# Optimization experiments

Measured on AMD Instinct MI355X. Metric: run time of the kernel, lower is better.

## Reference

```python
import jax, jax.numpy as jnp
import numpy as np

C_RADIUS = 20.0  # weighted-L1 ball radius from the cvxpy constraint
EPS = 1e-30


def weighted_l1_ball_projection(q, w, c):
    """Euclidean projection of each row of q onto {x : sum_i w_i*|x_i| <= c}, w>=0.
    Closed-form via sorted breakpoints: x_i = sign(q_i)*max(|q_i| - lam*w_i, 0).
    q, w: [B, D].
    """
    aq = jnp.abs(q)
    wa = w * aq                               # w_i |q_i|
    feasible = jnp.sum(wa, axis=-1) <= c      # already inside the ball
    # breakpoint ratios; coords with w==0 are never clipped -> push to the end
    r = jnp.where(w > 0, aq / jnp.maximum(w, EPS), -jnp.inf)
    order = jnp.argsort(-r, axis=-1)
    wa_s = jnp.take_along_axis(wa, order, axis=-1)
    w2_s = jnp.take_along_axis(w * w, order, axis=-1)
    r_s = jnp.take_along_axis(r, order, axis=-1)
    A = jnp.cumsum(wa_s, axis=-1)             # prefix sums over candidate active sets
    B = jnp.cumsum(w2_s, axis=-1)
    lam_k = (A - c) / jnp.maximum(B, EPS)
    valid = r_s > lam_k                       # active-set condition
    k = jnp.sum(valid, axis=-1)               # size of true active set
    idx = jnp.maximum(k - 1, 0)
    lam = jnp.take_along_axis(lam_k, idx[:, None], axis=-1)[:, 0]
    lam = jnp.where(feasible, 0.0, jnp.maximum(lam, 0.0))
    return jnp.sign(q) * jnp.maximum(aq - lam[:, None] * w, 0.0)


def setup_inputs() -> dict:
    key = jax.random.key(0)
    ks = jax.random.split(key, 8)
    state_dim, action_dim, B = 17, 6, 262144
    # scale state so the weighted-L1 constraint is occasionally active
    state = 4.0 * jax.random.normal(ks[0], (B, state_dim), dtype=jnp.float32)
    def lin(kw, kb, fan_out, fan_in):
        bound = 1.0 / np.sqrt(fan_in)
        W = jax.random.uniform(kw, (fan_out, fan_in), jnp.float32, -bound, bound)
        b = jax.random.uniform(kb, (fan_out,), jnp.float32, -bound, bound)
        return W, b
    l1_w, l1_b = lin(ks[1], ks[2], 400, state_dim)
    l2_w, l2_b = lin(ks[3], ks[4], 300, 400)
    l3_w, l3_b = lin(ks[5], ks[6], action_dim, 300)
    return {"state": state, "l1_w": l1_w, "l1_b": l1_b, "l2_w": l2_w,
            "l2_b": l2_b, "l3_w": l3_w, "l3_b": l3_b, "training": 0}


def reference(state, l1_w, l1_b, l2_w, l2_b, l3_w, l3_b, training):
    max_action = 1.0
    a = jax.nn.relu(state @ l1_w.T + l1_b)
    a = jax.nn.relu(a @ l2_w.T + l2_b)
    scaled_a = max_action * jnp.tanh(a @ l3_w.T + l3_b)  # [B, 6]
    # IS_TRAINING path: QP  min 0.5||x||^2 - q^T x  s.t. sum |x_i * s[11+i]| <= 20
    w = jnp.abs(state[:, 11:17])
    return weighted_l1_ball_projection(scaled_a, w, C_RADIUS)
```

## Files before the change

kernel.cpp:

```cpp
#include <hip/hip_runtime.h>
#include <math.h>

typedef _Float16 half2v __attribute__((ext_vector_type(2)));
typedef __fp16 fp16x2 __attribute__((ext_vector_type(2)));
typedef _Float16 half4 __attribute__((ext_vector_type(4)));
typedef _Float16 half8 __attribute__((ext_vector_type(8)));
typedef float floatx4 __attribute__((ext_vector_type(4)));

#define C_RADIUS 20.0f


__global__ void actor_prep(const float* __restrict__ w1, const float* __restrict__ b1,
                           const float* __restrict__ w2, const float* __restrict__ b2,
                           const float* __restrict__ w3, const float* __restrict__ b3,
                           _Float16* __restrict__ ws) {
  int gid = blockIdx.x * 256 + threadIdx.x;
  if (gid >= 19072) return;
  half8 hv;
  _Float16* dst;
  if (gid < 1792) {
    int l = gid & 63, tn = gid >> 6;
    int n = tn * 16 + (l & 15);
    int kc = 8 * (l >> 4);
#pragma unroll
    for (int e = 0; e < 8; ++e) {
      int k = kc + e;
      float v = 0.f;
      if (n < 400) {
        if (k < 17) v = w1[n * 17 + k];
        else if (k == 17) v = b1[n];
      }
      hv[e] = (_Float16)v;
    }
    dst = ws + gid * 8;
  } else if (gid < 1792 + 16640) {
    int g = gid - 1792;
    int l = g & 63, t = g >> 6;
    int ks = t % 13, tn = t / 13;
    int n = tn * 16 + (l & 15);
    int kc = ks * 32 + 8 * (l >> 4);
#pragma unroll
    for (int e = 0; e < 8; ++e) {
      int k = kc + e;
      float v = 0.f;
      if (n < 300) {
        if (k < 400) v = w2[n * 400 + k];
        else if (k == 400) v = b2[n];
      }
      hv[e] = (_Float16)v;
    }
    dst = ws + 14336 + g * 8;
  } else {
    int g = gid - 1792 - 16640;
    int l = g & 63, ks = g >> 6;
    int n = l & 15;
    int kc = ks * 32 + 8 * (l >> 4);
#pragma unroll
    for (int e = 0; e < 8; ++e) {
      int k = kc + e;
      float v = 0.f;
      if (n < 6) {
        if (k < 300) v = w3[n * 300 + k];
        else if (k == 300) v = b3[n];
      }
      hv[e] = (_Float16)v;
    }
    dst = ws + 147456 + g * 8;
  }
  *reinterpret_cast<half8*>(dst) = hv;
}

#define LD1 424
#define LD2 328
#define LDS_ 40

#define MFMA32(A, B, C) C = __builtin_amdgcn_mfma_f32_16x16x32_f16(A, B, C, 0, 0, 0)

__device__ __forceinline__ half4 pack4(float v0, float v1, float v2, float v3) {
  fp16x2 a = __builtin_amdgcn_cvt_pkrtz(v0, v1);
  fp16x2 b = __builtin_amdgcn_cvt_pkrtz(v2, v3);
  half2v a2 = __builtin_bit_cast(half2v, a);
  half2v b2 = __builtin_bit_cast(half2v, b);
  return __builtin_shufflevector(a2, b2, 0, 1, 2, 3);
}

__device__ __forceinline__ float fast_tanh(float x) {
  float e = __expf(2.0f * x);
  return 1.0f - 2.0f / (e + 1.0f);
}

__global__ __launch_bounds__(512, 4) void actor_fused(const float* __restrict__ state,
                                                      const _Float16* __restrict__ ws,
                                                      float* __restrict__ out) {
  __shared__ __align__(16) _Float16 aL[64 * LD1];
  __shared__ __align__(16) _Float16 stateF[64 * LDS_];
  __shared__ float z3L[64 * 8];
  __shared__ __align__(16) float outL[64 * 6];
  __shared__ float wvL[64 * 6];

  const int tid = threadIdx.x;
  const int lane = tid & 63;
  const int w = tid >> 6;
  const int r15 = lane & 15;
  const int c4 = lane >> 4;
  const int row0 = blockIdx.x * 64;

  for (int i = tid; i < 1088; i += 512) {
    int r = i / 17, c = i - r * 17;
    stateF[r * LDS_ + c] = (_Float16)state[row0 * 17 + i];
  }
  for (int i = tid; i < 64 * 23; i += 512) {
    int r = i / 23, c = 17 + (i - r * 23);
    stateF[r * LDS_ + c] = (c == 17) ? (_Float16)1.0f : (_Float16)0.0f;
  }
  for (int i = tid; i < 1024; i += 512) {
    int r = i >> 4, c = i & 15;
    aL[r * LD1 + 400 + c] = (c == 0) ? (_Float16)1.0f : (_Float16)0.0f;
  }
  if (tid < 384) {
    int r = tid / 6, c = tid - r * 6;
    wvL[tid] = fabsf(state[(row0 + r) * 17 + 11 + c]);
  }
  __syncthreads();

  {
    half8 S[4];
#pragma unroll
    for (int m = 0; m < 4; ++m)
      S[m] = *reinterpret_cast<const half8*>(&stateF[(16 * m + r15) * LDS_ + 8 * c4]);
    const half8* W1f = reinterpret_cast<const half8*>(ws);
#pragma unroll
    for (int t = 0; t < 4; ++t) {
      int tn = w + 8 * t;
      if (tn < 25) {
        half8 aW = W1f[tn * 64 + lane];
        floatx4 acc[4];
#pragma unroll
        for (int m = 0; m < 4; ++m) {
          acc[m] = (floatx4){0.f, 0.f, 0.f, 0.f};
          MFMA32(aW, S[m], acc[m]);
        }
        int n0 = tn * 16 + 4 * c4;
#pragma unroll
        for (int m = 0; m < 4; ++m) {
          half4 hv = pack4(fmaxf(acc[m][0], 0.f), fmaxf(acc[m][1], 0.f),
                           fmaxf(acc[m][2], 0.f), fmaxf(acc[m][3], 0.f));
          *reinterpret_cast<half4*>(&aL[(16 * m + r15) * LD1 + n0]) = hv;
        }
      }
    }
  }
  __syncthreads();

  {
    const half8* W2f = reinterpret_cast<const half8*>(ws + 14336);
    const int nt = (w < 4) ? 3 : 2;
    const int tn0 = (w < 4) ? (w * 3) : (12 + (w - 4) * 2);
    floatx4 acc[4][3];
#pragma unroll
    for (int m = 0; m < 4; ++m)
#pragma unroll
      for (int t = 0; t < 3; ++t) acc[m][t] = (floatx4){0.f, 0.f, 0.f, 0.f};

    half8 bX[3], bY[3];
#pragma unroll
    for (int t = 0; t < 3; ++t)
      if (t < nt) bX[t] = W2f[((tn0 + t) * 13 + 0) * 64 + lane];

#pragma unroll 1
    for (int ks = 0; ks < 13; ++ks) {
      if (ks < 12) {
#pragma unroll
        for (int t = 0; t < 3; ++t)
          if (t < nt) bY[t] = W2f[((tn0 + t) * 13 + ks + 1) * 64 + lane];
      }
      half8 F[4];
#pragma unroll
      for (int m = 0; m < 4; ++m)
        F[m] = *reinterpret_cast<const half8*>(&aL[(16 * m + r15) * LD1 + ks * 32 + 8 * c4]);
#pragma unroll
      for (int t = 0; t < 3; ++t)
        if (t < nt)
#pragma unroll
          for (int m = 0; m < 4; ++m)
            MFMA32(bX[t], F[m], acc[m][t]);
#pragma unroll
      for (int t = 0; t < 3; ++t) bX[t] = bY[t];
    }
    __syncthreads();

#pragma unroll
    for (int t = 0; t < 3; ++t)
      if (t < nt) {
        int n0 = (tn0 + t) * 16 + 4 * c4;
#pragma unroll
        for (int m = 0; m < 4; ++m) {
          float v0 = fmaxf(acc[m][t][0], 0.f), v1 = fmaxf(acc[m][t][1], 0.f);
          float v2 = fmaxf(acc[m][t][2], 0.f), v3 = fmaxf(acc[m][t][3], 0.f);
          if (n0 == 300) v0 = 1.0f;
          half4 hv = pack4(v0, v1, v2, v3);
          *reinterpret_cast<half4*>(&aL[(16 * m + r15) * LD2 + n0]) = hv;
        }
      }
  }
  __syncthreads();

  if (w < 4) {
    const half8* W3f = reinterpret_cast<const half8*>(ws + 147456);
    floatx4 za = (floatx4){0.f, 0.f, 0.f, 0.f};
    floatx4 zb = (floatx4){0.f, 0.f, 0.f, 0.f};
    const int row = 16 * w + r15;
#pragma unroll
    for (int ks = 0; ks < 10; ks += 2) {
      half8 F0 = *reinterpret_cast<const half8*>(&aL[row * LD2 + ks * 32 + 8 * c4]);
      half8 F1 = *reinterpret_cast<const half8*>(&aL[row * LD2 + (ks + 1) * 32 + 8 * c4]);
      MFMA32(W3f[ks * 64 + lane], F0, za);
      MFMA32(W3f[(ks + 1) * 64 + lane], F1, zb);
    }
    floatx4 z = za + zb;
    if (c4 == 0) {
#pragma unroll
      for (int j = 0; j < 4; ++j) z3L[row * 8 + j] = fast_tanh(z[j]);
    } else if (c4 == 1) {
      z3L[row * 8 + 4] = fast_tanh(z[0]);
      z3L[row * 8 + 5] = fast_tanh(z[1]);
    }
  }
  __syncthreads();

  if (tid < 64) {
    const int row = tid;
    float q[6], wv[6], aq[6], wa[6];
    float S = 0.f;
#pragma unroll
    for (int i = 0; i < 6; ++i) {
      q[i] = z3L[row * 8 + i];
      wv[i] = wvL[row * 6 + i];
      aq[i] = fabsf(q[i]);
      wa[i] = wv[i] * aq[i];
      S += wa[i];
    }
    float lam = 0.f;
    if (!(S <= C_RADIUS)) {
      float rr[6], w2s[6], was[6];
#pragma unroll
      for (int i = 0; i < 6; ++i) {
        rr[i] = (wv[i] > 0.f) ? (aq[i] / fmaxf(wv[i], 1e-30f)) : -__builtin_inff();
        w2s[i] = wv[i] * wv[i];
        was[i] = wa[i];
      }
#pragma unroll
      for (int p = 0; p < 5; ++p)
#pragma unroll
        for (int j2 = 0; j2 < 5; ++j2)
          if (j2 < 5 - p) {
            if (rr[j2] < rr[j2 + 1]) {
              float t0 = rr[j2];  rr[j2] = rr[j2 + 1];  rr[j2 + 1] = t0;
              float t1 = w2s[j2]; w2s[j2] = w2s[j2 + 1]; w2s[j2 + 1] = t1;
              float t2 = was[j2]; was[j2] = was[j2 + 1]; was[j2 + 1] = t2;
            }
          }
      float A = 0.f, Bc = 0.f;
      float lamk[6];
      int kc = 0;
#pragma unroll
      for (int i = 0; i < 6; ++i) {
        A += was[i];
        Bc += w2s[i];
        lamk[i] = (A - C_RADIUS) / fmaxf(Bc, 1e-30f);
        if (rr[i] > lamk[i]) ++kc;
      }
      int idx = kc - 1;
      if (idx < 0) idx = 0;
      float lsel = lamk[0];
#pragma unroll
      for (int i = 1; i < 6; ++i)
        if (i == idx) lsel = lamk[i];
      lam = fmaxf(lsel, 0.f);
    }
#pragma unroll
    for (int i = 0; i < 6; ++i) {
      float x = fmaxf(aq[i] - lam * wv[i], 0.f);
      outL[row * 6 + i] = copysignf(x, q[i]);
    }
  }
  __syncthreads();

  if (tid < 96) {
    float4 v = reinterpret_cast<const float4*>(outL)[tid];
    reinterpret_cast<float4*>(out)[blockIdx.x * 96 + tid] = v;
  }
}

extern "C" void kernel_launch(void* const* d_in, const int* in_sizes, int n_in,
                              void* d_out, int out_size, void* d_ws, size_t ws_size,
                              hipStream_t stream) {
  const float* state = (const float*)d_in[0];
  const float* w1 = (const float*)d_in[1];
  const float* b1 = (const float*)d_in[2];
  const float* w2 = (const float*)d_in[3];
  const float* b2 = (const float*)d_in[4];
  const float* w3 = (const float*)d_in[5];
  const float* b3 = (const float*)d_in[6];
  _Float16* ws = (_Float16*)d_ws;
  float* out = (float*)d_out;

  actor_prep<<<75, 256, 0, stream>>>(w1, b1, w2, b2, w3, b3, ws);
  actor_fused<<<4096, 512, 0, stream>>>(state, ws, out);
}
```

Baseline: 97.10 us.

## Trim LDS footprint, fold state into aL pad, raise occupancy, fuse projection tail

Drops the separate stateF, z3L, outL and wvL shared buffers. The state tile now goes into the padding columns of aL, and the layer-2 bias is added in the epilogue instead of through a constant-one column, so the smaller LDS footprint allows launch bounds of 6 blocks. The layer-2 K loop is restructured into ping-pong register buffers, and the first weight load is issued before layer 1. The QP projection now runs directly in the layer-3 wave using shuffles, which removes two barriers and the staged output write, at the cost of higher register pressure and uncoalesced per-row stores.

```diff
diff --git a/kernel.cpp b/kernel.cpp
--- a/kernel.cpp
+++ b/kernel.cpp
@@ -43,10 +43,7 @@
     for (int e = 0; e < 8; ++e) {
       int k = kc + e;
       float v = 0.f;
-      if (n < 300) {
-        if (k < 400) v = w2[n * 400 + k];
-        else if (k == 400) v = b2[n];
-      }
+      if (n < 300 && k < 400) v = w2[n * 400 + k];
       hv[e] = (_Float16)v;
     }
     dst = ws + 14336 + g * 8;
@@ -72,7 +69,6 @@
 
 #define LD1 424
 #define LD2 328
-#define LDS_ 40
 
 #define MFMA32(A, B, C) C = __builtin_amdgcn_mfma_f32_16x16x32_f16(A, B, C, 0, 0, 0)
 
@@ -89,14 +85,11 @@
   return 1.0f - 2.0f / (e + 1.0f);
 }
 
-__global__ __launch_bounds__(512, 4) void actor_fused(const float* __restrict__ state,
+__global__ __launch_bounds__(512, 6) void actor_fused(const float* __restrict__ state,
                                                       const _Float16* __restrict__ ws,
+                                                      const float* __restrict__ b2,
                                                       float* __restrict__ out) {
   __shared__ __align__(16) _Float16 aL[64 * LD1];
-  __shared__ __align__(16) _Float16 stateF[64 * LDS_];
-  __shared__ float z3L[64 * 8];
-  __shared__ __align__(16) float outL[64 * 6];
-  __shared__ float wvL[64 * 6];
 
   const int tid = threadIdx.x;
   const int lane = tid & 63;
@@ -105,29 +98,32 @@
   const int c4 = lane >> 4;
   const int row0 = blockIdx.x * 64;
 
-  for (int i = tid; i < 1088; i += 512) {
-    int r = i / 17, c = i - r * 17;
-    stateF[r * LDS_ + c] = (_Float16)state[row0 * 17 + i];
-  }
-  for (int i = tid; i < 64 * 23; i += 512) {
-    int r = i / 23, c = 17 + (i - r * 23);
-    stateF[r * LDS_ + c] = (c == 17) ? (_Float16)1.0f : (_Float16)0.0f;
-  }
-  for (int i = tid; i < 1024; i += 512) {
-    int r = i >> 4, c = i & 15;
-    aL[r * LD1 + 400 + c] = (c == 0) ? (_Float16)1.0f : (_Float16)0.0f;
-  }
-  if (tid < 384) {
-    int r = tid / 6, c = tid - r * 6;
-    wvL[tid] = fabsf(state[(row0 + r) * 17 + 11 + c]);
+  for (int i = tid; i < 1536; i += 512) {
+    int r = i / 24, c = i - r * 24;
+    float v = 0.f;
+    if (c < 17) v = state[(row0 + r) * 17 + c];
+    else if (c == 17) v = 1.0f;
+    aL[r * LD1 + 400 + c] = (_Float16)v;
   }
   __syncthreads();
+
+  const int nt = (w < 4) ? 3 : 2;
+  const int tn0 = (w < 4) ? (w * 3) : (12 + (w - 4) * 2);
+  const half8* W2f = reinterpret_cast<const half8*>(ws + 14336);
+  half8 bA[3], bB[3];
+#pragma unroll
+  for (int t = 0; t < 3; ++t)
+    if (t < nt) bA[t] = W2f[((tn0 + t) * 13 + 0) * 64 + lane];
 
   {
     half8 S[4];
 #pragma unroll
-    for (int m = 0; m < 4; ++m)
-      S[m] = *reinterpret_cast<const half8*>(&stateF[(16 * m + r15) * LDS_ + 8 * c4]);
+    for (int m = 0; m < 4; ++m) {
+      half8 v = {};
+      if (c4 < 3)
+        v = *reinterpret_cast<const half8*>(&aL[(16 * m + r15) * LD1 + 400 + 8 * c4]);
+      S[m] = v;
+    }
     const half8* W1f = reinterpret_cast<const half8*>(ws);
 #pragma unroll
     for (int t = 0; t < 4; ++t) {
@@ -153,50 +149,65 @@
   __syncthreads();
 
   {
-    const half8* W2f = reinterpret_cast<const half8*>(ws + 14336);
-    const int nt = (w < 4) ? 3 : 2;
-    const int tn0 = (w < 4) ? (w * 3) : (12 + (w - 4) * 2);
     floatx4 acc[4][3];
 #pragma unroll
     for (int m = 0; m < 4; ++m)
 #pragma unroll
       for (int t = 0; t < 3; ++t) acc[m][t] = (floatx4){0.f, 0.f, 0.f, 0.f};
 
-    half8 bX[3], bY[3];
-#pragma unroll
-    for (int t = 0; t < 3; ++t)
-      if (t < nt) bX[t] = W2f[((tn0 + t) * 13 + 0) * 64 + lane];
+    const int n0base = tn0 * 16 + 4 * c4;
+    float4 b2v[3];
+#pragma unroll
+    for (int t = 0; t < 3; ++t) {
+      b2v[t] = make_float4(0.f, 0.f, 0.f, 0.f);
+      int n0 = n0base + 16 * t;
+      if (t < nt && n0 < 300) b2v[t] = *reinterpret_cast<const float4*>(&b2[n0]);
+    }
 
 #pragma unroll 1
-    for (int ks = 0; ks < 13; ++ks) {
-      if (ks < 12) {
+    for (int kp = 0; kp < 6; ++kp) {
+      const int ks0 = 2 * kp, ks1 = 2 * kp + 1, ks2 = 2 * kp + 2;
+#pragma unroll
+      for (int t = 0; t < 3; ++t)
+        if (t < nt) bB[t] = W2f[((tn0 + t) * 13 + ks1) * 64 + lane];
+#pragma unroll
+      for (int m = 0; m < 4; ++m) {
+        half8 F = *reinterpret_cast<const half8*>(&aL[(16 * m + r15) * LD1 + ks0 * 32 + 8 * c4]);
 #pragma unroll
         for (int t = 0; t < 3; ++t)
-          if (t < nt) bY[t] = W2f[((tn0 + t) * 13 + ks + 1) * 64 + lane];
-      }
-      half8 F[4];
-#pragma unroll
-      for (int m = 0; m < 4; ++m)
-        F[m] = *reinterpret_cast<const half8*>(&aL[(16 * m + r15) * LD1 + ks * 32 + 8 * c4]);
+          if (t < nt) MFMA32(bA[t], F, acc[m][t]);
+      }
 #pragma unroll
       for (int t = 0; t < 3; ++t)
-        if (t < nt)
-#pragma unroll
-          for (int m = 0; m < 4; ++m)
-            MFMA32(bX[t], F[m], acc[m][t]);
-#pragma unroll
-      for (int t = 0; t < 3; ++t) bX[t] = bY[t];
-    }
+        if (t < nt) bA[t] = W2f[((tn0 + t) * 13 + ks2) * 64 + lane];
+#pragma unroll
+      for (int m = 0; m < 4; ++m) {
+        half8 F = *reinterpret_cast<const half8*>(&aL[(16 * m + r15) * LD1 + ks1 * 32 + 8 * c4]);
+#pragma unroll
+        for (int t = 0; t < 3; ++t)
+          if (t < nt) MFMA32(bB[t], F, acc[m][t]);
+      }
+    }
+#pragma unroll
+    for (int m = 0; m < 4; ++m) {
+      half8 F = *reinterpret_cast<const half8*>(&aL[(16 * m + r15) * LD1 + 12 * 32 + 8 * c4]);
+#pragma unroll
+      for (int t = 0; t < 3; ++t)
+        if (t < nt) MFMA32(bA[t], F, acc[m][t]);
+    }
+
     __syncthreads();
 
 #pragma unroll
     for (int t = 0; t < 3; ++t)
       if (t < nt) {
-        int n0 = (tn0 + t) * 16 + 4 * c4;
+        int n0 = n0base + 16 * t;
 #pragma unroll
         for (int m = 0; m < 4; ++m) {
-          float v0 = fmaxf(acc[m][t][0], 0.f), v1 = fmaxf(acc[m][t][1], 0.f);
-          float v2 = fmaxf(acc[m][t][2], 0.f), v3 = fmaxf(acc[m][t][3], 0.f);
+          float v0 = fmaxf(acc[m][t][0] + b2v[t].x, 0.f);
+          float v1 = fmaxf(acc[m][t][1] + b2v[t].y, 0.f);
+          float v2 = fmaxf(acc[m][t][2] + b2v[t].z, 0.f);
+          float v3 = fmaxf(acc[m][t][3] + b2v[t].w, 0.f);
           if (n0 == 300) v0 = 1.0f;
           half4 hv = pack4(v0, v1, v2, v3);
           *reinterpret_cast<half4*>(&aL[(16 * m + r15) * LD2 + n0]) = hv;
@@ -218,77 +229,66 @@
       MFMA32(W3f[(ks + 1) * 64 + lane], F1, zb);
     }
     floatx4 z = za + zb;
+    float v4 = __shfl(z[0], r15 + 16, 64);
+    float v5 = __shfl(z[1], r15 + 16, 64);
     if (c4 == 0) {
-#pragma unroll
-      for (int j = 0; j < 4; ++j) z3L[row * 8 + j] = fast_tanh(z[j]);
-    } else if (c4 == 1) {
-      z3L[row * 8 + 4] = fast_tanh(z[0]);
-      z3L[row * 8 + 5] = fast_tanh(z[1]);
-    }
-  }
-  __syncthreads();
-
-  if (tid < 64) {
-    const int row = tid;
-    float q[6], wv[6], aq[6], wa[6];
-    float S = 0.f;
-#pragma unroll
-    for (int i = 0; i < 6; ++i) {
-      q[i] = z3L[row * 8 + i];
-      wv[i] = wvL[row * 6 + i];
-      aq[i] = fabsf(q[i]);
-      wa[i] = wv[i] * aq[i];
-      S += wa[i];
-    }
-    float lam = 0.f;
-    if (!(S <= C_RADIUS)) {
-      float rr[6], w2s[6], was[6];
+      const int grow = row0 + row;
+      float q[6], wv[6], aq[6], wa[6];
+      q[0] = fast_tanh(z[0]); q[1] = fast_tanh(z[1]);
+      q[2] = fast_tanh(z[2]); q[3] = fast_tanh(z[3]);
+      q[4] = fast_tanh(v4);   q[5] = fast_tanh(v5);
+      float S = 0.f;
 #pragma unroll
       for (int i = 0; i < 6; ++i) {
-        rr[i] = (wv[i] > 0.f) ? (aq[i] / fmaxf(wv[i], 1e-30f)) : -__builtin_inff();
-        w2s[i] = wv[i] * wv[i];
-        was[i] = wa[i];
-      }
-#pragma unroll
-      for (int p = 0; p < 5; ++p)
-#pragma unroll
-        for (int j2 = 0; j2 < 5; ++j2)
-          if (j2 < 5 - p) {
-            if (rr[j2] < rr[j2 + 1]) {
-              float t0 = rr[j2];  rr[j2] = rr[j2 + 1];  rr[j2 + 1] = t0;
-              float t1 = w2s[j2]; w2s[j2] = w2s[j2 + 1]; w2s[j2 + 1] = t1;
-              float t2 = was[j2]; was[j2] = was[j2 + 1]; was[j2 + 1] = t2;
+        wv[i] = fabsf(state[grow * 17 + 11 + i]);
+        aq[i] = fabsf(q[i]);
+        wa[i] = wv[i] * aq[i];
+        S += wa[i];
+      }
+      float lam = 0.f;
+      if (!(S <= C_RADIUS)) {
+        float rr[6], w2s[6], was[6];
+#pragma unroll
+        for (int i = 0; i < 6; ++i) {
+          rr[i] = (wv[i] > 0.f) ? (aq[i] / fmaxf(wv[i], 1e-30f)) : -__builtin_inff();
+          w2s[i] = wv[i] * wv[i];
+          was[i] = wa[i];
+        }
+#pragma unroll
+        for (int p = 0; p < 5; ++p)
+#pragma unroll
+          for (int j2 = 0; j2 < 5; ++j2)
+            if (j2 < 5 - p) {
+              if (rr[j2] < rr[j2 + 1]) {
+                float t0 = rr[j2];  rr[j2] = rr[j2 + 1];  rr[j2 + 1] = t0;
+                float t1 = w2s[j2]; w2s[j2] = w2s[j2 + 1]; w2s[j2 + 1] = t1;
+                float t2 = was[j2]; was[j2] = was[j2 + 1]; was[j2 + 1] = t2;
+              }
             }
-          }
-      float A = 0.f, Bc = 0.f;
-      float lamk[6];
-      int kc = 0;
+        float A = 0.f, Bc = 0.f;
+        float lamk[6];
+        int kc = 0;
+#pragma unroll
+        for (int i = 0; i < 6; ++i) {
+          A += was[i];
+          Bc += w2s[i];
+          lamk[i] = (A - C_RADIUS) / fmaxf(Bc, 1e-30f);
+          if (rr[i] > lamk[i]) ++kc;
+        }
+        int idx = kc - 1;
+        if (idx < 0) idx = 0;
+        float lsel = lamk[0];
+#pragma unroll
+        for (int i = 1; i < 6; ++i)
+          if (i == idx) lsel = lamk[i];
+        lam = fmaxf(lsel, 0.f);
+      }
 #pragma unroll
       for (int i = 0; i < 6; ++i) {
-        A += was[i];
-        Bc += w2s[i];
-        lamk[i] = (A - C_RADIUS) / fmaxf(Bc, 1e-30f);
-        if (rr[i] > lamk[i]) ++kc;
-      }
-      int idx = kc - 1;
-      if (idx < 0) idx = 0;
-      float lsel = lamk[0];
-#pragma unroll
-      for (int i = 1; i < 6; ++i)
-        if (i == idx) lsel = lamk[i];
-      lam = fmaxf(lsel, 0.f);
-    }
-#pragma unroll
-    for (int i = 0; i < 6; ++i) {
-      float x = fmaxf(aq[i] - lam * wv[i], 0.f);
-      outL[row * 6 + i] = copysignf(x, q[i]);
-    }
-  }
-  __syncthreads();
-
-  if (tid < 96) {
-    float4 v = reinterpret_cast<const float4*>(outL)[tid];
-    reinterpret_cast<float4*>(out)[blockIdx.x * 96 + tid] = v;
+        float x = fmaxf(aq[i] - lam * wv[i], 0.f);
+        out[grow * 6 + i] = copysignf(x, q[i]);
+      }
+    }
   }
 }
 
@@ -306,5 +306,5 @@
   float* out = (float*)d_out;
 
   actor_prep<<<75, 256, 0, stream>>>(w1, b1, w2, b2, w3, b3, ws);
-  actor_fused<<<4096, 512, 0, stream>>>(state, ws, out);
-}
+  actor_fused<<<4096, 512, 0, stream>>>(state, ws, b2, out);
+}
```

After: 275.7 us. 2.84x slower.

## Shrink LDS footprint and fuse projection into layer-3 waves for higher occupancy

Applied to the files above, without the earlier changes.

Stages state directly into the activation LDS buffer (bias column moved to k=0), drops the separate stateF, z3L, outL and wvL buffers, and trims LD1 so more blocks fit per CU. Occupancy hint rises from 4 to 6. The weighted-L1 projection now runs in the layer-3 waves, using shuffles to gather outputs 4 and 5 and reading weights straight from global memory. This removes two barriers and the LDS round trips. The layer-2 weight prefetch is simplified from double-buffered registers to a single buffer loaded after the MFMAs. That lowers register pressure but exposes more global-load latency, and output stores are now per-thread scattered writes instead of coalesced float4.

```diff
diff --git a/kernel.cpp b/kernel.cpp
--- a/kernel.cpp
+++ b/kernel.cpp
@@ -27,8 +27,8 @@
       int k = kc + e;
       float v = 0.f;
       if (n < 400) {
-        if (k < 17) v = w1[n * 17 + k];
-        else if (k == 17) v = b1[n];
+        if (k == 0) v = b1[n];
+        else if (k <= 17) v = w1[n * 17 + (k - 1)];
       }
       hv[e] = (_Float16)v;
     }
@@ -70,9 +70,8 @@
   *reinterpret_cast<half8*>(dst) = hv;
 }
 
-#define LD1 424
+#define LD1 408
 #define LD2 328
-#define LDS_ 40
 
 #define MFMA32(A, B, C) C = __builtin_amdgcn_mfma_f32_16x16x32_f16(A, B, C, 0, 0, 0)
 
@@ -89,14 +88,10 @@
   return 1.0f - 2.0f / (e + 1.0f);
 }
 
-__global__ __launch_bounds__(512, 4) void actor_fused(const float* __restrict__ state,
+__global__ __launch_bounds__(512, 6) void actor_fused(const float* __restrict__ state,
                                                       const _Float16* __restrict__ ws,
                                                       float* __restrict__ out) {
-  __shared__ __align__(16) _Float16 aL[64 * LD1];
-  __shared__ __align__(16) _Float16 stateF[64 * LDS_];
-  __shared__ float z3L[64 * 8];
-  __shared__ __align__(16) float outL[64 * 6];
-  __shared__ float wvL[64 * 6];
+  __shared__ __align__(16) _Float16 aL[64 * LD1 + 16];
 
   const int tid = threadIdx.x;
   const int lane = tid & 63;
@@ -105,29 +100,27 @@
   const int c4 = lane >> 4;
   const int row0 = blockIdx.x * 64;
 
-  for (int i = tid; i < 1088; i += 512) {
-    int r = i / 17, c = i - r * 17;
-    stateF[r * LDS_ + c] = (_Float16)state[row0 * 17 + i];
-  }
-  for (int i = tid; i < 64 * 23; i += 512) {
-    int r = i / 23, c = 17 + (i - r * 23);
-    stateF[r * LDS_ + c] = (c == 17) ? (_Float16)1.0f : (_Float16)0.0f;
-  }
-  for (int i = tid; i < 1024; i += 512) {
-    int r = i >> 4, c = i & 15;
+  for (int i = tid; i < 2048; i += 512) {
+    int r = i >> 5, c = i & 31;
+    float v = 0.f;
+    if (c == 0) v = 1.0f;
+    else if (c <= 17) v = state[(row0 + r) * 17 + (c - 1)];
+    aL[r * LD1 + c] = (_Float16)v;
+  }
+  {
+    int r = tid >> 3, c = tid & 7;
     aL[r * LD1 + 400 + c] = (c == 0) ? (_Float16)1.0f : (_Float16)0.0f;
   }
-  if (tid < 384) {
-    int r = tid / 6, c = tid - r * 6;
-    wvL[tid] = fabsf(state[(row0 + r) * 17 + 11 + c]);
-  }
+  if (tid < 16) aL[64 * LD1 + tid] = (_Float16)0.0f;
+  __syncthreads();
+
+  half8 S[4];
+#pragma unroll
+  for (int m = 0; m < 4; ++m)
+    S[m] = *reinterpret_cast<const half8*>(&aL[(16 * m + r15) * LD1 + 8 * c4]);
   __syncthreads();
 
   {
-    half8 S[4];
-#pragma unroll
-    for (int m = 0; m < 4; ++m)
-      S[m] = *reinterpret_cast<const half8*>(&stateF[(16 * m + r15) * LDS_ + 8 * c4]);
     const half8* W1f = reinterpret_cast<const half8*>(ws);
 #pragma unroll
     for (int t = 0; t < 4; ++t) {
@@ -162,18 +155,13 @@
 #pragma unroll
       for (int t = 0; t < 3; ++t) acc[m][t] = (floatx4){0.f, 0.f, 0.f, 0.f};
 
-    half8 bX[3], bY[3];
+    half8 bA[3];
 #pragma unroll
     for (int t = 0; t < 3; ++t)
-      if (t < nt) bX[t] = W2f[((tn0 + t) * 13 + 0) * 64 + lane];
+      if (t < nt) bA[t] = W2f[((tn0 + t) * 13 + 0) * 64 + lane];
 
 #pragma unroll 1
     for (int ks = 0; ks < 13; ++ks) {
-      if (ks < 12) {
-#pragma unroll
-        for (int t = 0; t < 3; ++t)
-          if (t < nt) bY[t] = W2f[((tn0 + t) * 13 + ks + 1) * 64 + lane];
-      }
       half8 F[4];
 #pragma unroll
       for (int m = 0; m < 4; ++m)
@@ -183,10 +171,14 @@
         if (t < nt)
 #pragma unroll
           for (int m = 0; m < 4; ++m)
-            MFMA32(bX[t], F[m], acc[m][t]);
-#pragma unroll
-      for (int t = 0; t < 3; ++t) bX[t] = bY[t];
-    }
+            MFMA32(bA[t], F[m], acc[m][t]);
+      if (ks < 12) {
+#pragma unroll
+        for (int t = 0; t < 3; ++t)
+          if (t < nt) bA[t] = W2f[((tn0 + t) * 13 + ks + 1) * 64 + lane];
+      }
+    }
+
     __syncthreads();
 
 #pragma unroll
@@ -218,77 +210,66 @@
       MFMA32(W3f[(ks + 1) * 64 + lane], F1, zb);
     }
     floatx4 z = za + zb;
+    float v4 = __shfl(z[0], r15 + 16, 64);
+    float v5 = __shfl(z[1], r15 + 16, 64);
     if (c4 == 0) {
-#pragma unroll
-      for (int j = 0; j < 4; ++j) z3L[row * 8 + j] = fast_tanh(z[j]);
-    } else if (c4 == 1) {
-      z3L[row * 8 + 4] = fast_tanh(z[0]);
-      z3L[row * 8 + 5] = fast_tanh(z[1]);
-    }
-  }
-  __syncthreads();
-
-  if (tid < 64) {
-    const int row = tid;
-    float q[6], wv[6], aq[6], wa[6];
-    float S = 0.f;
-#pragma unroll
-    for (int i = 0; i < 6; ++i) {
-      q[i] = z3L[row * 8 + i];
-      wv[i] = wvL[row * 6 + i];
-      aq[i] = fabsf(q[i]);
-      wa[i] = wv[i] * aq[i];
-      S += wa[i];
-    }
-    float lam = 0.f;
-    if (!(S <= C_RADIUS)) {
-      float rr[6], w2s[6], was[6];
+      const int grow = row0 + row;
+      float q[6], wv[6], aq[6], wa[6];
+      q[0] = fast_tanh(z[0]); q[1] = fast_tanh(z[1]);
+      q[2] = fast_tanh(z[2]); q[3] = fast_tanh(z[3]);
+      q[4] = fast_tanh(v4);   q[5] = fast_tanh(v5);
+      float S2 = 0.f;
 #pragma unroll
       for (int i = 0; i < 6; ++i) {
-        rr[i] = (wv[i] > 0.f) ? (aq[i] / fmaxf(wv[i], 1e-30f)) : -__builtin_inff();
-        w2s[i] = wv[i] * wv[i];
-        was[i] = wa[i];
-      }
-#pragma unroll
-      for (int p = 0; p < 5; ++p)
-#pragma unroll
-        for (int j2 = 0; j2 < 5; ++j2)
-          if (j2 < 5 - p) {
-            if (rr[j2] < rr[j2 + 1]) {
-              float t0 = rr[j2];  rr[j2] = rr[j2 + 1];  rr[j2 + 1] = t0;
-              float t1 = w2s[j2]; w2s[j2] = w2s[j2 + 1]; w2s[j2 + 1] = t1;
-              float t2 = was[j2]; was[j2] = was[j2 + 1]; was[j2 + 1] = t2;
+        wv[i] = fabsf(state[grow * 17 + 11 + i]);
+        aq[i] = fabsf(q[i]);
+        wa[i] = wv[i] * aq[i];
+        S2 += wa[i];
+      }
+      float lam = 0.f;
+      if (!(S2 <= C_RADIUS)) {
+        float rr[6], w2s[6], was[6];
+#pragma unroll
+        for (int i = 0; i < 6; ++i) {
+          rr[i] = (wv[i] > 0.f) ? (aq[i] / fmaxf(wv[i], 1e-30f)) : -__builtin_inff();
+          w2s[i] = wv[i] * wv[i];
+          was[i] = wa[i];
+        }
+#pragma unroll
+        for (int p = 0; p < 5; ++p)
+#pragma unroll
+          for (int j2 = 0; j2 < 5; ++j2)
+            if (j2 < 5 - p) {
+              if (rr[j2] < rr[j2 + 1]) {
+                float t0 = rr[j2];  rr[j2] = rr[j2 + 1];  rr[j2 + 1] = t0;
+                float t1 = w2s[j2]; w2s[j2] = w2s[j2 + 1]; w2s[j2 + 1] = t1;
+                float t2 = was[j2]; was[j2] = was[j2 + 1]; was[j2 + 1] = t2;
+              }
             }
-          }
-      float A = 0.f, Bc = 0.f;
-      float lamk[6];
-      int kc = 0;
+        float A = 0.f, Bc = 0.f;
+        float lamk[6];
+        int kc = 0;
+#pragma unroll
+        for (int i = 0; i < 6; ++i) {
+          A += was[i];
+          Bc += w2s[i];
+          lamk[i] = (A - C_RADIUS) / fmaxf(Bc, 1e-30f);
+          if (rr[i] > lamk[i]) ++kc;
+        }
+        int idx = kc - 1;
+        if (idx < 0) idx = 0;
+        float lsel = lamk[0];
+#pragma unroll
+        for (int i = 1; i < 6; ++i)
+          if (i == idx) lsel = lamk[i];
+        lam = fmaxf(lsel, 0.f);
+      }
 #pragma unroll
       for (int i = 0; i < 6; ++i) {
-        A += was[i];
-        Bc += w2s[i];
-        lamk[i] = (A - C_RADIUS) / fmaxf(Bc, 1e-30f);
-        if (rr[i] > lamk[i]) ++kc;
-      }
-      int idx = kc - 1;
-      if (idx < 0) idx = 0;
-      float lsel = lamk[0];
-#pragma unroll
-      for (int i = 1; i < 6; ++i)
-        if (i == idx) lsel = lamk[i];
-      lam = fmaxf(lsel, 0.f);
-    }
-#pragma unroll
-    for (int i = 0; i < 6; ++i) {
-      float x = fmaxf(aq[i] - lam * wv[i], 0.f);
-      outL[row * 6 + i] = copysignf(x, q[i]);
-    }
-  }
-  __syncthreads();
-
-  if (tid < 96) {
-    float4 v = reinterpret_cast<const float4*>(outL)[tid];
-    reinterpret_cast<float4*>(out)[blockIdx.x * 96 + tid] = v;
+        float x = fmaxf(aq[i] - lam * wv[i], 0.f);
+        out[grow * 6 + i] = copysignf(x, q[i]);
+      }
+    }
   }
 }
 
```

Result: faster. 92.96 us (-4.3%).
